# Performance work log

Measured on AMD Instinct MI355X. Metric: run time of the kernel, lower is better.

## Reference

```python
import jax, jax.numpy as jnp
import numpy as np

B, S, D, H = 2, 2048, 1024, 16
DK = D // H


def setup_inputs() -> dict:
    key = jax.random.key(0)
    ks = jax.random.split(key, 8)
    w_scale = 1.0 / np.sqrt(D)
    return {
        "query": jax.random.normal(ks[0], (B, S, D), jnp.float32),
        "key": jax.random.normal(ks[1], (B, S, D), jnp.float32),
        "value": jax.random.normal(ks[2], (B, S, D), jnp.float32),
        "Wq": jax.random.normal(ks[3], (D, D), jnp.float32) * w_scale,
        "bq": jnp.zeros((D,), jnp.float32),
        "Wk": jax.random.normal(ks[4], (D, D), jnp.float32) * w_scale,
        "bk": jnp.zeros((D,), jnp.float32),
        "Wv": jax.random.normal(ks[5], (D, D), jnp.float32) * w_scale,
        "bv": jnp.zeros((D,), jnp.float32),
        "Wo": jax.random.normal(ks[6], (D, D), jnp.float32) * w_scale,
        "bo": jnp.zeros((D,), jnp.float32),
    }


def _heads(x, W, b):
    # torch nn.Linear: y = x @ W.T + b ; then [B,S,D] -> [B,H,S,DK]
    y = x @ W.T + b
    return y.reshape(x.shape[0], x.shape[1], H, DK).transpose(0, 2, 1, 3)


def reference(query, key, value, Wq, bq, Wk, bk, Wv, bv, Wo, bo):
    q = _heads(query, Wq, bq)   # [B,H,S,DK]
    k = _heads(key, Wk, bk)
    v = _heads(value, Wv, bv)
    scale = 100.0 / np.sqrt(DK).astype(np.float32)
    scores = jnp.einsum("bhqd,bhkd->bhqk", q, k) * scale  # [B,H,Sq,Sk]
    prob = jax.nn.softmax(scores, axis=-1)                 # dropout p=0 -> identity
    out = jnp.einsum("bhqk,bhkd->bhqd", prob, v)           # [B,H,Sq,DK]
    mean_atp = prob.mean(axis=(1, 2))                      # mean over heads & query -> [B,Sk]
    out = out.transpose(0, 2, 1, 3).reshape(query.shape[0], -1, D)
    out = out @ Wo.T + bo
    return out, mean_atp
```

## Files before the change

### kernel.cpp

```cpp
#include <hip/hip_runtime.h>
#include <hip/hip_bf16.h>


#define B_  2
#define S_  2048
#define D_  1024
#define H_  16
#define DK_ 64

typedef __bf16 bf16x8 __attribute__((ext_vector_type(8)));
typedef float f32x4  __attribute__((ext_vector_type(4)));

__device__ __forceinline__ void ld_g2l16(const __bf16* g, __bf16* l) {
  __builtin_amdgcn_global_load_lds(
      (const __attribute__((address_space(1))) void*)g,
      (__attribute__((address_space(3))) void*)l, 16, 0, 0);
}

__device__ __forceinline__ void split3_body(const float* __restrict__ x,
                                            __bf16* __restrict__ y,
                                            int lbid, int tid, int mode)
{
  int i = (lbid * 256 + tid) * 8;
  float4 a = *(const float4*)(x + i);
  float4 b = *(const float4*)(x + i + 4);
  float xs[8] = {a.x, a.y, a.z, a.w, b.x, b.y, b.z, b.w};
  __bf16 out[24];
#pragma unroll
  for (int j = 0; j < 8; j++) {
    float v = xs[j];
    __bf16 hi = (__bf16)v;
    __bf16 lo = (__bf16)(v - (float)hi);
    if (mode == 0) { out[3*j] = hi; out[3*j+1] = hi; out[3*j+2] = lo; }
    else           { out[3*j] = hi; out[3*j+1] = lo; out[3*j+2] = hi; }
  }
  *(bf16x8*)(y + 3 * (size_t)i)      = *(bf16x8*)&out[0];
  *(bf16x8*)(y + 3 * (size_t)i + 8)  = *(bf16x8*)&out[8];
  *(bf16x8*)(y + 3 * (size_t)i + 16) = *(bf16x8*)&out[16];
}

__device__ __forceinline__ void tobf16_body(const float* __restrict__ x,
                                            __bf16* __restrict__ y,
                                            int lbid, int tid)
{
  int i = (lbid * 256 + tid) * 8;
  float4 a = *(const float4*)(x + i);
  float4 b = *(const float4*)(x + i + 4);
  __bf16 out[8] = {(__bf16)a.x, (__bf16)a.y, (__bf16)a.z, (__bf16)a.w,
                   (__bf16)b.x, (__bf16)b.y, (__bf16)b.z, (__bf16)b.w};
  *(bf16x8*)(y + i) = *(bf16x8*)&out[0];
}

__global__ __launch_bounds__(256)
void convert_all(const float* __restrict__ query, const float* __restrict__ key_,
                 const float* __restrict__ value, const float* __restrict__ Wq,
                 const float* __restrict__ Wk, const float* __restrict__ Wv,
                 const float* __restrict__ Wo, __bf16* __restrict__ qcat3,
                 __bf16* __restrict__ kcat3, __bf16* __restrict__ vxb,
                 __bf16* __restrict__ wqc3, __bf16* __restrict__ wkc3,
                 __bf16* __restrict__ wvb, __bf16* __restrict__ wob)
{
  int bid = blockIdx.x, tid = threadIdx.x;
  if (bid < 2048)       split3_body(query, qcat3, bid, tid, 0);
  else if (bid < 4096)  split3_body(key_,  kcat3, bid - 2048, tid, 0);
  else if (bid < 6144)  tobf16_body(value, vxb,   bid - 4096, tid);
  else if (bid < 6656)  split3_body(Wq, wqc3, bid - 6144, tid, 1);
  else if (bid < 7168)  split3_body(Wk, wkc3, bid - 6656, tid, 1);
  else if (bid < 7680)  tobf16_body(Wv, wvb, bid - 7168, tid);
  else                  tobf16_body(Wo, wob, bid - 7680, tid);
}

#define TM 64
#define TN 128
#define TK 64

__global__ __launch_bounds__(256)
void gemm_mfma(const __bf16* __restrict__ X, const __bf16* __restrict__ W,
               const float* __restrict__ bias, void* __restrict__ Y,
               void* __restrict__ Y2, int M, int N, int K, int out_mode,
               float osf)
{
  __shared__ __align__(16) __bf16 Xa[TM * TK];
  __shared__ __align__(16) __bf16 Wb[TN * TK];

  const int tid  = threadIdx.x;
  const int lane = tid & 63;
  const int w    = tid >> 6;
  const int c    = lane & 15;
  const int quad = lane >> 4;
  const int row0 = blockIdx.y * TM;
  const int col0 = blockIdx.x * TN;
  const int wc   = w * 32;

  f32x4 acc[4][2];
#pragma unroll
  for (int i = 0; i < 4; i++)
#pragma unroll
    for (int j = 0; j < 2; j++) acc[i][j] = (f32x4){0.f, 0.f, 0.f, 0.f};

  for (int k0 = 0; k0 < K; k0 += TK) {
    __syncthreads();
#pragma unroll
    for (int i = 0; i < 2; i++) {
      int chunk = i * 256 + w * 64 + lane;
      int r = chunk >> 3, dch = chunk & 7;
      ld_g2l16(X + (size_t)(row0 + r) * K + k0 + dch * 8, &Xa[chunk * 8]);
    }
#pragma unroll
    for (int i = 0; i < 4; i++) {
      int chunk = i * 256 + w * 64 + lane;
      int r = chunk >> 3, dch = chunk & 7;
      ld_g2l16(W + (size_t)(col0 + r) * K + k0 + dch * 8, &Wb[chunk * 8]);
    }
    __syncthreads();

#pragma unroll
    for (int cc = 0; cc < 2; cc++) {
      bf16x8 af[4], bf[2];
#pragma unroll
      for (int i = 0; i < 4; i++)
        af[i] = *(const bf16x8*)&Xa[(i * 16 + c) * TK + cc * 32 + quad * 8];
#pragma unroll
      for (int j = 0; j < 2; j++)
        bf[j] = *(const bf16x8*)&Wb[(wc + j * 16 + c) * TK + cc * 32 + quad * 8];
#pragma unroll
      for (int i = 0; i < 4; i++)
#pragma unroll
        for (int j = 0; j < 2; j++)
          acc[i][j] = __builtin_amdgcn_mfma_f32_16x16x32_bf16(af[i], bf[j],
                                                              acc[i][j], 0, 0, 0);
    }
  }

#pragma unroll
  for (int i = 0; i < 4; i++) {
#pragma unroll
    for (int j = 0; j < 2; j++) {
      int col = col0 + wc + j * 16 + c;
      float bcol = bias[col];
#pragma unroll
      for (int r = 0; r < 4; r++) {
        int row = row0 + i * 16 + quad * 4 + r;
        float v = (acc[i][j][r] + bcol) * osf;
        if (out_mode == 0) {
          ((float*)Y)[(size_t)row * N + col] = v;
        } else {
          int b2 = row >> 11, s = row & (S_ - 1);
          int h = col >> 6, dk = col & 63;
          if (out_mode == 1) {
            size_t off = ((size_t)(b2 * H_ + h) * S_ + s) * DK_ + dk;
            __bf16 hi = (__bf16)v;
            ((__bf16*)Y)[off]  = hi;
            ((__bf16*)Y2)[off] = (__bf16)(v - (float)hi);
          } else {
            ((__bf16*)Y)[((size_t)(b2 * H_ + h) * DK_ + dk) * S_ + s] = (__bf16)v;
          }
        }
      }
    }
  }
}

#define LSTR 72
#define PSTR 68

__device__ __forceinline__ void qk_scores(const __bf16* __restrict__ Kh,
                                          const __bf16* __restrict__ Kl,
                                          const bf16x8 qhf[2][2],
                                          const bf16x8 qlf[2][2],
                                          int c, int quad, f32x4 sc[2][4])
{
#pragma unroll
  for (int nt = 0; nt < 4; nt++) {
#pragma unroll
    for (int rg = 0; rg < 2; rg++) sc[rg][nt] = (f32x4){0.f, 0.f, 0.f, 0.f};
#pragma unroll
    for (int cc = 0; cc < 2; cc++) {
      bf16x8 bh8 = *(const bf16x8*)&Kh[(nt * 16 + c) * LSTR + cc * 32 + quad * 8];
      bf16x8 bl8 = *(const bf16x8*)&Kl[(nt * 16 + c) * LSTR + cc * 32 + quad * 8];
#pragma unroll
      for (int rg = 0; rg < 2; rg++) {
        sc[rg][nt] = __builtin_amdgcn_mfma_f32_16x16x32_bf16(qhf[rg][cc], bh8,
                                                             sc[rg][nt], 0, 0, 0);
        sc[rg][nt] = __builtin_amdgcn_mfma_f32_16x16x32_bf16(qhf[rg][cc], bl8,
                                                             sc[rg][nt], 0, 0, 0);
        sc[rg][nt] = __builtin_amdgcn_mfma_f32_16x16x32_bf16(qlf[rg][cc], bh8,
                                                             sc[rg][nt], 0, 0, 0);
      }
    }
  }
}

__global__ __launch_bounds__(256)
void attn_mfma(const __bf16* __restrict__ qh_ws, const __bf16* __restrict__ ql_ws,
               const __bf16* __restrict__ kh_ws, const __bf16* __restrict__ kl_ws,
               const __bf16* __restrict__ vt_ws, __bf16* __restrict__ attn_out,
               float* __restrict__ atp_out)
{
  __shared__ __align__(16) __bf16 Kh[64 * LSTR];
  __shared__ __align__(16) __bf16 Kl[64 * LSTR];
  __shared__ __align__(16) __bf16 Vt[64 * LSTR];
  __shared__ __align__(16) float  Ps[4][16 * PSTR];
  __shared__ float  atp_lds[S_];

  const int tid  = threadIdx.x;
  const int lane = tid & 63;
  const int w    = tid >> 6;
  const int c    = lane & 15;
  const int quad = lane >> 4;
  const int qb   = blockIdx.x;
  const int h    = blockIdx.y;
  const int b    = blockIdx.z;

  const size_t bh = (size_t)(b * H_ + h);
  const __bf16* qhg = qh_ws + (bh * S_ + qb * 128) * DK_;
  const __bf16* qlg = ql_ws + (bh * S_ + qb * 128) * DK_;
  const __bf16* khg = kh_ws + bh * S_ * DK_;
  const __bf16* klg = kl_ws + bh * S_ * DK_;
  const __bf16* vg  = vt_ws + bh * DK_ * S_;

  bf16x8 qhf[2][2], qlf[2][2];
#pragma unroll
  for (int rg = 0; rg < 2; rg++) {
    const __bf16* qrow = qhg + (size_t)(w * 32 + rg * 16 + c) * DK_;
    qhf[rg][0] = *(const bf16x8*)(qrow + quad * 8);
    qhf[rg][1] = *(const bf16x8*)(qrow + 32 + quad * 8);
    const __bf16* qrow2 = qlg + (size_t)(w * 32 + rg * 16 + c) * DK_;
    qlf[rg][0] = *(const bf16x8*)(qrow2 + quad * 8);
    qlf[rg][1] = *(const bf16x8*)(qrow2 + 32 + quad * 8);
  }

  float m_r[2][4], l_r[2][4];
#pragma unroll
  for (int rg = 0; rg < 2; rg++)
#pragma unroll
    for (int r = 0; r < 4; r++) { m_r[rg][r] = -1e30f; l_r[rg][r] = 0.f; }

  for (int kt = 0; kt < S_ / 64; kt++) {
    __syncthreads();
#pragma unroll
    for (int i = 0; i < 2; i++) {
      int idx = i * 256 + tid;
      int key = idx >> 3, dch = idx & 7;
      *(bf16x8*)&Kh[key * LSTR + dch * 8] =
          *(const bf16x8*)(khg + (size_t)(kt * 64 + key) * DK_ + dch * 8);
      *(bf16x8*)&Kl[key * LSTR + dch * 8] =
          *(const bf16x8*)(klg + (size_t)(kt * 64 + key) * DK_ + dch * 8);
    }
    __syncthreads();

    f32x4 sc[2][4];
    qk_scores(Kh, Kl, qhf, qlf, c, quad, sc);

    float tm[2][4], psum[2][4];
#pragma unroll
    for (int rg = 0; rg < 2; rg++)
#pragma unroll
      for (int r = 0; r < 4; r++)
        tm[rg][r] = fmaxf(fmaxf(sc[rg][0][r], sc[rg][1][r]),
                          fmaxf(sc[rg][2][r], sc[rg][3][r]));
#pragma unroll
    for (int o = 1; o < 16; o <<= 1)
#pragma unroll
      for (int rg = 0; rg < 2; rg++)
#pragma unroll
        for (int r = 0; r < 4; r++)
          tm[rg][r] = fmaxf(tm[rg][r], __shfl_xor(tm[rg][r], o, 64));

#pragma unroll
    for (int rg = 0; rg < 2; rg++)
#pragma unroll
      for (int r = 0; r < 4; r++) {
        float mnew = fmaxf(m_r[rg][r], tm[rg][r]);
        float p = 0.f;
#pragma unroll
        for (int nt = 0; nt < 4; nt++) p += exp2f(sc[rg][nt][r] - mnew);
        psum[rg][r] = p;
        l_r[rg][r] *= exp2f(m_r[rg][r] - mnew);
        m_r[rg][r] = mnew;
      }
#pragma unroll
    for (int o = 1; o < 16; o <<= 1)
#pragma unroll
      for (int rg = 0; rg < 2; rg++)
#pragma unroll
        for (int r = 0; r < 4; r++)
          psum[rg][r] += __shfl_xor(psum[rg][r], o, 64);
#pragma unroll
    for (int rg = 0; rg < 2; rg++)
#pragma unroll
      for (int r = 0; r < 4; r++) l_r[rg][r] += psum[rg][r];
  }

  float rl[2][4];
#pragma unroll
  for (int rg = 0; rg < 2; rg++)
#pragma unroll
    for (int r = 0; r < 4; r++) rl[rg][r] = 1.0f / l_r[rg][r];

  for (int i = tid; i < S_; i += 256) atp_lds[i] = 0.f;

  f32x4 of[2][4];
#pragma unroll
  for (int rg = 0; rg < 2; rg++)
#pragma unroll
    for (int nt = 0; nt < 4; nt++) of[rg][nt] = (f32x4){0.f, 0.f, 0.f, 0.f};

  float* ps = Ps[w];

  for (int kt = 0; kt < S_ / 64; kt++) {
    __syncthreads();
#pragma unroll
    for (int i = 0; i < 2; i++) {
      int idx = i * 256 + tid;
      int key = idx >> 3, dch = idx & 7;
      *(bf16x8*)&Kh[key * LSTR + dch * 8] =
          *(const bf16x8*)(khg + (size_t)(kt * 64 + key) * DK_ + dch * 8);
      *(bf16x8*)&Kl[key * LSTR + dch * 8] =
          *(const bf16x8*)(klg + (size_t)(kt * 64 + key) * DK_ + dch * 8);
      *(bf16x8*)&Vt[key * LSTR + dch * 8] =
          *(const bf16x8*)(vg + (size_t)key * S_ + kt * 64 + dch * 8);
    }
    __syncthreads();

    f32x4 sc[2][4];
    qk_scores(Kh, Kl, qhf, qlf, c, quad, sc);

    float t[4] = {0.f, 0.f, 0.f, 0.f};
#pragma unroll
    for (int rg = 0; rg < 2; rg++) {
#pragma unroll
      for (int nt = 0; nt < 4; nt++)
#pragma unroll
        for (int r = 0; r < 4; r++) {
          float p = exp2f(sc[rg][nt][r] - m_r[rg][r]) * rl[rg][r];
          ps[(quad * 4 + r) * PSTR + nt * 16 + c] = p;
          t[nt] += p;
        }
      bf16x8 pa[2];
#pragma unroll
      for (int cc = 0; cc < 2; cc++) {
        const float* pp = &ps[c * PSTR + cc * 32 + quad * 8];
        f32x4 p0 = *(const f32x4*)pp;
        f32x4 p1 = *(const f32x4*)(pp + 4);
        bf16x8 v8;
#pragma unroll
        for (int j = 0; j < 4; j++) { v8[j] = (__bf16)p0[j]; v8[4 + j] = (__bf16)p1[j]; }
        pa[cc] = v8;
      }
#pragma unroll
      for (int nt = 0; nt < 4; nt++)
#pragma unroll
        for (int cc = 0; cc < 2; cc++) {
          bf16x8 vb = *(const bf16x8*)&Vt[(nt * 16 + c) * LSTR + cc * 32 + quad * 8];
          of[rg][nt] = __builtin_amdgcn_mfma_f32_16x16x32_bf16(pa[cc], vb,
                                                               of[rg][nt], 0, 0, 0);
        }
    }

#pragma unroll
    for (int nt = 0; nt < 4; nt++) {
      float tt = t[nt];
      tt += __shfl_xor(tt, 16, 64);
      tt += __shfl_xor(tt, 32, 64);
      if (quad == 0) atomicAdd(&atp_lds[kt * 64 + nt * 16 + c], tt);
    }
  }

#pragma unroll
  for (int rg = 0; rg < 2; rg++)
#pragma unroll
    for (int nt = 0; nt < 4; nt++)
#pragma unroll
      for (int r = 0; r < 4; r++)
        attn_out[((size_t)(b * S_ + qb * 128 + w * 32 + rg * 16 + quad * 4 + r)) * D_
                 + h * DK_ + nt * 16 + c] = (__bf16)of[rg][nt][r];

  __syncthreads();
  const float inv = 1.0f / ((float)H_ * (float)S_);
  for (int i = tid; i < S_; i += 256)
    atomicAdd(&atp_out[b * S_ + i], atp_lds[i] * inv);
}

__global__ void zero_f32(float* __restrict__ p, int n) {
  int i = blockIdx.x * 256 + threadIdx.x;
  if (i < n) p[i] = 0.f;
}

extern "C" void kernel_launch(void* const* d_in, const int* in_sizes, int n_in,
                              void* d_out, int out_size, void* d_ws, size_t ws_size,
                              hipStream_t stream)
{
  const float* query = (const float*)d_in[0];
  const float* key_  = (const float*)d_in[1];
  const float* value = (const float*)d_in[2];
  const float* Wq = (const float*)d_in[3];
  const float* bq = (const float*)d_in[4];
  const float* Wk = (const float*)d_in[5];
  const float* bk = (const float*)d_in[6];
  const float* Wv = (const float*)d_in[7];
  const float* bv = (const float*)d_in[8];
  const float* Wo = (const float*)d_in[9];
  const float* bo = (const float*)d_in[10];

  float* out = (float*)d_out;
  float* atp = out + (size_t)B_ * S_ * D_;

  const size_t NE = (size_t)B_ * S_ * D_;
  const size_t NW = (size_t)D_ * D_;
  __bf16* p = (__bf16*)d_ws;
  __bf16* qcat3 = p;               p += 3 * NE;
  __bf16* kcat3 = p;               p += 3 * NE;
  __bf16* wqc3  = p;               p += 3 * NW;
  __bf16* wkc3  = p;               p += 3 * NW;
  __bf16* vxb   = p;               p += NE;
  __bf16* wvb   = p;               p += NW;
  __bf16* wob   = p;               p += NW;
  __bf16* qh_ws = p;               p += NE;
  __bf16* ql_ws = p;               p += NE;
  __bf16* kh_ws = p;               p += NE;
  __bf16* kl_ws = p;               p += NE;
  __bf16* vt_ws = kcat3;
  __bf16* a_ws  = qcat3;

  const int M = B_ * S_;
  const float QSF = 18.0337320f;

  convert_all<<<8192, 256, 0, stream>>>(query, key_, value, Wq, Wk, Wv, Wo,
                                        qcat3, kcat3, vxb, wqc3, wkc3, wvb, wob);

  dim3 ggrid(D_ / TN, M / TM);
  gemm_mfma<<<ggrid, 256, 0, stream>>>(qcat3, wqc3, bq, qh_ws, ql_ws, M, D_, 3 * D_, 1, QSF);
  gemm_mfma<<<ggrid, 256, 0, stream>>>(kcat3, wkc3, bk, kh_ws, kl_ws, M, D_, 3 * D_, 1, 1.0f);
  gemm_mfma<<<ggrid, 256, 0, stream>>>(vxb,   wvb,  bv, vt_ws, nullptr, M, D_, D_, 2, 1.0f);

  zero_f32<<<(B_ * S_ + 255) / 256, 256, 0, stream>>>(atp, B_ * S_);

  attn_mfma<<<dim3(S_ / 128, H_, B_), 256, 0, stream>>>(qh_ws, ql_ws, kh_ws, kl_ws,
                                                        vt_ws, a_ws, atp);

  gemm_mfma<<<ggrid, 256, 0, stream>>>(a_ws, wob, bo, out, nullptr, M, D_, D_, 0, 1.0f);
}
```

Before: 511.3 us.

## Merge QKV GEMMs into one launch, fold atp zeroing, use 8-wave attention blocks

```diff
diff --git a/kernel.cpp b/kernel.cpp
--- a/kernel.cpp
+++ b/kernel.cpp
@@ -58,7 +58,8 @@
                  const float* __restrict__ Wo, __bf16* __restrict__ qcat3,
                  __bf16* __restrict__ kcat3, __bf16* __restrict__ vxb,
                  __bf16* __restrict__ wqc3, __bf16* __restrict__ wkc3,
-                 __bf16* __restrict__ wvb, __bf16* __restrict__ wob)
+                 __bf16* __restrict__ wvb, __bf16* __restrict__ wob,
+                 float* __restrict__ atp)
 {
   int bid = blockIdx.x, tid = threadIdx.x;
   if (bid < 2048)       split3_body(query, qcat3, bid, tid, 0);
@@ -67,29 +68,31 @@
   else if (bid < 6656)  split3_body(Wq, wqc3, bid - 6144, tid, 1);
   else if (bid < 7168)  split3_body(Wk, wkc3, bid - 6656, tid, 1);
   else if (bid < 7680)  tobf16_body(Wv, wvb, bid - 7168, tid);
-  else                  tobf16_body(Wo, wob, bid - 7680, tid);
+  else if (bid < 8192)  tobf16_body(Wo, wob, bid - 7680, tid);
+  else {
+    int base = (bid - 8192) * 2048;
+#pragma unroll
+    for (int j = 0; j < 8; j++) atp[base + j * 256 + tid] = 0.f;
+  }
 }
 
 #define TM 64
 #define TN 128
 #define TK 64
 
-__global__ __launch_bounds__(256)
-void gemm_mfma(const __bf16* __restrict__ X, const __bf16* __restrict__ W,
+__device__ __forceinline__
+void gemm_body(const __bf16* __restrict__ X, const __bf16* __restrict__ W,
                const float* __restrict__ bias, void* __restrict__ Y,
-               void* __restrict__ Y2, int M, int N, int K, int out_mode,
-               float osf)
-{
-  __shared__ __align__(16) __bf16 Xa[TM * TK];
-  __shared__ __align__(16) __bf16 Wb[TN * TK];
-
+               void* __restrict__ Y2, int N, int K, int out_mode, float osf,
+               __bf16* Xa, __bf16* Wb, int bx, int by)
+{
   const int tid  = threadIdx.x;
   const int lane = tid & 63;
   const int w    = tid >> 6;
   const int c    = lane & 15;
   const int quad = lane >> 4;
-  const int row0 = blockIdx.y * TM;
-  const int col0 = blockIdx.x * TN;
+  const int row0 = by * TM;
+  const int col0 = bx * TN;
   const int wc   = w * 32;
 
   f32x4 acc[4][2];
@@ -161,37 +164,60 @@
   }
 }
 
+__global__ __launch_bounds__(256)
+void gemm_qkv(const __bf16* __restrict__ qcat3, const __bf16* __restrict__ wqc3,
+              const float* __restrict__ bq, __bf16* __restrict__ qh, __bf16* __restrict__ ql,
+              const __bf16* __restrict__ kcat3, const __bf16* __restrict__ wkc3,
+              const float* __restrict__ bk, __bf16* __restrict__ kh, __bf16* __restrict__ kl,
+              const __bf16* __restrict__ vxb, const __bf16* __restrict__ wvb,
+              const float* __restrict__ bv, __bf16* __restrict__ vt, float qsf)
+{
+  __shared__ __align__(16) __bf16 Xa[TM * TK];
+  __shared__ __align__(16) __bf16 Wb[TN * TK];
+  int z = blockIdx.z;
+  if (z == 0)
+    gemm_body(qcat3, wqc3, bq, qh, ql, D_, 3 * D_, 1, qsf, Xa, Wb, blockIdx.x, blockIdx.y);
+  else if (z == 1)
+    gemm_body(kcat3, wkc3, bk, kh, kl, D_, 3 * D_, 1, 1.0f, Xa, Wb, blockIdx.x, blockIdx.y);
+  else
+    gemm_body(vxb, wvb, bv, vt, nullptr, D_, D_, 2, 1.0f, Xa, Wb, blockIdx.x, blockIdx.y);
+}
+
+__global__ __launch_bounds__(256)
+void gemm_mfma(const __bf16* __restrict__ X, const __bf16* __restrict__ W,
+               const float* __restrict__ bias, void* __restrict__ Y,
+               void* __restrict__ Y2, int M, int N, int K, int out_mode,
+               float osf)
+{
+  __shared__ __align__(16) __bf16 Xa[TM * TK];
+  __shared__ __align__(16) __bf16 Wb[TN * TK];
+  gemm_body(X, W, bias, Y, Y2, N, K, out_mode, osf, Xa, Wb, blockIdx.x, blockIdx.y);
+}
+
 #define LSTR 72
 #define PSTR 68
 
 __device__ __forceinline__ void qk_scores(const __bf16* __restrict__ Kh,
                                           const __bf16* __restrict__ Kl,
-                                          const bf16x8 qhf[2][2],
-                                          const bf16x8 qlf[2][2],
-                                          int c, int quad, f32x4 sc[2][4])
+                                          const bf16x8 qhf[2],
+                                          const bf16x8 qlf[2],
+                                          int c, int quad, f32x4 sc[4])
 {
 #pragma unroll
   for (int nt = 0; nt < 4; nt++) {
-#pragma unroll
-    for (int rg = 0; rg < 2; rg++) sc[rg][nt] = (f32x4){0.f, 0.f, 0.f, 0.f};
+    sc[nt] = (f32x4){0.f, 0.f, 0.f, 0.f};
 #pragma unroll
     for (int cc = 0; cc < 2; cc++) {
       bf16x8 bh8 = *(const bf16x8*)&Kh[(nt * 16 + c) * LSTR + cc * 32 + quad * 8];
       bf16x8 bl8 = *(const bf16x8*)&Kl[(nt * 16 + c) * LSTR + cc * 32 + quad * 8];
-#pragma unroll
-      for (int rg = 0; rg < 2; rg++) {
-        sc[rg][nt] = __builtin_amdgcn_mfma_f32_16x16x32_bf16(qhf[rg][cc], bh8,
-                                                             sc[rg][nt], 0, 0, 0);
-        sc[rg][nt] = __builtin_amdgcn_mfma_f32_16x16x32_bf16(qhf[rg][cc], bl8,
-                                                             sc[rg][nt], 0, 0, 0);
-        sc[rg][nt] = __builtin_amdgcn_mfma_f32_16x16x32_bf16(qlf[rg][cc], bh8,
-                                                             sc[rg][nt], 0, 0, 0);
-      }
-    }
-  }
-}
-
-__global__ __launch_bounds__(256)
+      sc[nt] = __builtin_amdgcn_mfma_f32_16x16x32_bf16(qhf[cc], bh8, sc[nt], 0, 0, 0);
+      sc[nt] = __builtin_amdgcn_mfma_f32_16x16x32_bf16(qhf[cc], bl8, sc[nt], 0, 0, 0);
+      sc[nt] = __builtin_amdgcn_mfma_f32_16x16x32_bf16(qlf[cc], bh8, sc[nt], 0, 0, 0);
+    }
+  }
+}
+
+__global__ __launch_bounds__(512)
 void attn_mfma(const __bf16* __restrict__ qh_ws, const __bf16* __restrict__ ql_ws,
                const __bf16* __restrict__ kh_ws, const __bf16* __restrict__ kl_ws,
                const __bf16* __restrict__ vt_ws, __bf16* __restrict__ attn_out,
@@ -200,7 +226,7 @@
   __shared__ __align__(16) __bf16 Kh[64 * LSTR];
   __shared__ __align__(16) __bf16 Kl[64 * LSTR];
   __shared__ __align__(16) __bf16 Vt[64 * LSTR];
-  __shared__ __align__(16) float  Ps[4][16 * PSTR];
+  __shared__ __align__(16) float  Ps[8][16 * PSTR];
   __shared__ float  atp_lds[S_];
 
   const int tid  = threadIdx.x;
@@ -219,29 +245,24 @@
   const __bf16* klg = kl_ws + bh * S_ * DK_;
   const __bf16* vg  = vt_ws + bh * DK_ * S_;
 
-  bf16x8 qhf[2][2], qlf[2][2];
-#pragma unroll
-  for (int rg = 0; rg < 2; rg++) {
-    const __bf16* qrow = qhg + (size_t)(w * 32 + rg * 16 + c) * DK_;
-    qhf[rg][0] = *(const bf16x8*)(qrow + quad * 8);
-    qhf[rg][1] = *(const bf16x8*)(qrow + 32 + quad * 8);
-    const __bf16* qrow2 = qlg + (size_t)(w * 32 + rg * 16 + c) * DK_;
-    qlf[rg][0] = *(const bf16x8*)(qrow2 + quad * 8);
-    qlf[rg][1] = *(const bf16x8*)(qrow2 + 32 + quad * 8);
-  }
-
-  float m_r[2][4], l_r[2][4];
-#pragma unroll
-  for (int rg = 0; rg < 2; rg++)
-#pragma unroll
-    for (int r = 0; r < 4; r++) { m_r[rg][r] = -1e30f; l_r[rg][r] = 0.f; }
+  bf16x8 qhf[2], qlf[2];
+  {
+    const __bf16* qrow = qhg + (size_t)(w * 16 + c) * DK_;
+    qhf[0] = *(const bf16x8*)(qrow + quad * 8);
+    qhf[1] = *(const bf16x8*)(qrow + 32 + quad * 8);
+    const __bf16* qrow2 = qlg + (size_t)(w * 16 + c) * DK_;
+    qlf[0] = *(const bf16x8*)(qrow2 + quad * 8);
+    qlf[1] = *(const bf16x8*)(qrow2 + 32 + quad * 8);
+  }
+
+  float m_r[4], l_r[4];
+#pragma unroll
+  for (int r = 0; r < 4; r++) { m_r[r] = -1e30f; l_r[r] = 0.f; }
 
   for (int kt = 0; kt < S_ / 64; kt++) {
     __syncthreads();
-#pragma unroll
-    for (int i = 0; i < 2; i++) {
-      int idx = i * 256 + tid;
-      int key = idx >> 3, dch = idx & 7;
+    {
+      int key = tid >> 3, dch = tid & 7;
       *(bf16x8*)&Kh[key * LSTR + dch * 8] =
           *(const bf16x8*)(khg + (size_t)(kt * 64 + key) * DK_ + dch * 8);
       *(bf16x8*)&Kl[key * LSTR + dch * 8] =
@@ -249,71 +270,54 @@
     }
     __syncthreads();
 
-    f32x4 sc[2][4];
+    f32x4 sc[4];
     qk_scores(Kh, Kl, qhf, qlf, c, quad, sc);
 
-    float tm[2][4], psum[2][4];
-#pragma unroll
-    for (int rg = 0; rg < 2; rg++)
+    float tm[4], psum[4];
+#pragma unroll
+    for (int r = 0; r < 4; r++)
+      tm[r] = fmaxf(fmaxf(sc[0][r], sc[1][r]), fmaxf(sc[2][r], sc[3][r]));
+#pragma unroll
+    for (int o = 1; o < 16; o <<= 1)
 #pragma unroll
       for (int r = 0; r < 4; r++)
-        tm[rg][r] = fmaxf(fmaxf(sc[rg][0][r], sc[rg][1][r]),
-                          fmaxf(sc[rg][2][r], sc[rg][3][r]));
+        tm[r] = fmaxf(tm[r], __shfl_xor(tm[r], o, 64));
+
+#pragma unroll
+    for (int r = 0; r < 4; r++) {
+      float mnew = fmaxf(m_r[r], tm[r]);
+      float p = 0.f;
+#pragma unroll
+      for (int nt = 0; nt < 4; nt++) p += exp2f(sc[nt][r] - mnew);
+      psum[r] = p;
+      l_r[r] *= exp2f(m_r[r] - mnew);
+      m_r[r] = mnew;
+    }
 #pragma unroll
     for (int o = 1; o < 16; o <<= 1)
 #pragma unroll
-      for (int rg = 0; rg < 2; rg++)
-#pragma unroll
-        for (int r = 0; r < 4; r++)
-          tm[rg][r] = fmaxf(tm[rg][r], __shfl_xor(tm[rg][r], o, 64));
-
-#pragma unroll
-    for (int rg = 0; rg < 2; rg++)
-#pragma unroll
-      for (int r = 0; r < 4; r++) {
-        float mnew = fmaxf(m_r[rg][r], tm[rg][r]);
-        float p = 0.f;
-#pragma unroll
-        for (int nt = 0; nt < 4; nt++) p += exp2f(sc[rg][nt][r] - mnew);
-        psum[rg][r] = p;
-        l_r[rg][r] *= exp2f(m_r[rg][r] - mnew);
-        m_r[rg][r] = mnew;
-      }
-#pragma unroll
-    for (int o = 1; o < 16; o <<= 1)
-#pragma unroll
-      for (int rg = 0; rg < 2; rg++)
-#pragma unroll
-        for (int r = 0; r < 4; r++)
-          psum[rg][r] += __shfl_xor(psum[rg][r], o, 64);
-#pragma unroll
-    for (int rg = 0; rg < 2; rg++)
-#pragma unroll
-      for (int r = 0; r < 4; r++) l_r[rg][r] += psum[rg][r];
-  }
-
-  float rl[2][4];
-#pragma unroll
-  for (int rg = 0; rg < 2; rg++)
-#pragma unroll
-    for (int r = 0; r < 4; r++) rl[rg][r] = 1.0f / l_r[rg][r];
-
-  for (int i = tid; i < S_; i += 256) atp_lds[i] = 0.f;
-
-  f32x4 of[2][4];
-#pragma unroll
-  for (int rg = 0; rg < 2; rg++)
-#pragma unroll
-    for (int nt = 0; nt < 4; nt++) of[rg][nt] = (f32x4){0.f, 0.f, 0.f, 0.f};
+      for (int r = 0; r < 4; r++)
+        psum[r] += __shfl_xor(psum[r], o, 64);
+#pragma unroll
+    for (int r = 0; r < 4; r++) l_r[r] += psum[r];
+  }
+
+  float z_r[4];
+#pragma unroll
+  for (int r = 0; r < 4; r++) z_r[r] = m_r[r] + log2f(l_r[r]);
+
+  for (int i = tid; i < S_; i += 512) atp_lds[i] = 0.f;
+
+  f32x4 of[4];
+#pragma unroll
+  for (int nt = 0; nt < 4; nt++) of[nt] = (f32x4){0.f, 0.f, 0.f, 0.f};
 
   float* ps = Ps[w];
 
   for (int kt = 0; kt < S_ / 64; kt++) {
     __syncthreads();
-#pragma unroll
-    for (int i = 0; i < 2; i++) {
-      int idx = i * 256 + tid;
-      int key = idx >> 3, dch = idx & 7;
+    {
+      int key = tid >> 3, dch = tid & 7;
       *(bf16x8*)&Kh[key * LSTR + dch * 8] =
           *(const bf16x8*)(khg + (size_t)(kt * 64 + key) * DK_ + dch * 8);
       *(bf16x8*)&Kl[key * LSTR + dch * 8] =
@@ -323,40 +327,39 @@
     }
     __syncthreads();
 
-    f32x4 sc[2][4];
+    f32x4 sc[4];
     qk_scores(Kh, Kl, qhf, qlf, c, quad, sc);
 
-    float t[4] = {0.f, 0.f, 0.f, 0.f};
-#pragma unroll
-    for (int rg = 0; rg < 2; rg++) {
-#pragma unroll
-      for (int nt = 0; nt < 4; nt++)
-#pragma unroll
-        for (int r = 0; r < 4; r++) {
-          float p = exp2f(sc[rg][nt][r] - m_r[rg][r]) * rl[rg][r];
-          ps[(quad * 4 + r) * PSTR + nt * 16 + c] = p;
-          t[nt] += p;
-        }
-      bf16x8 pa[2];
+    float t[4];
+#pragma unroll
+    for (int nt = 0; nt < 4; nt++) {
+      t[nt] = 0.f;
+#pragma unroll
+      for (int r = 0; r < 4; r++) {
+        float p = exp2f(sc[nt][r] - z_r[r]);
+        ps[(quad * 4 + r) * PSTR + nt * 16 + c] = p;
+        t[nt] += p;
+      }
+    }
+
+    bf16x8 pa[2];
+#pragma unroll
+    for (int cc = 0; cc < 2; cc++) {
+      const float* pp = &ps[c * PSTR + cc * 32 + quad * 8];
+      f32x4 p0 = *(const f32x4*)pp;
+      f32x4 p1 = *(const f32x4*)(pp + 4);
+      bf16x8 v8;
+#pragma unroll
+      for (int j = 0; j < 4; j++) { v8[j] = (__bf16)p0[j]; v8[4 + j] = (__bf16)p1[j]; }
+      pa[cc] = v8;
+    }
+#pragma unroll
+    for (int nt = 0; nt < 4; nt++)
 #pragma unroll
       for (int cc = 0; cc < 2; cc++) {
-        const float* pp = &ps[c * PSTR + cc * 32 + quad * 8];
-        f32x4 p0 = *(const f32x4*)pp;
-        f32x4 p1 = *(const f32x4*)(pp + 4);
-        bf16x8 v8;
-#pragma unroll
-        for (int j = 0; j < 4; j++) { v8[j] = (__bf16)p0[j]; v8[4 + j] = (__bf16)p1[j]; }
-        pa[cc] = v8;
+        bf16x8 vb = *(const bf16x8*)&Vt[(nt * 16 + c) * LSTR + cc * 32 + quad * 8];
+        of[nt] = __builtin_amdgcn_mfma_f32_16x16x32_bf16(pa[cc], vb, of[nt], 0, 0, 0);
       }
-#pragma unroll
-      for (int nt = 0; nt < 4; nt++)
-#pragma unroll
-        for (int cc = 0; cc < 2; cc++) {
-          bf16x8 vb = *(const bf16x8*)&Vt[(nt * 16 + c) * LSTR + cc * 32 + quad * 8];
-          of[rg][nt] = __builtin_amdgcn_mfma_f32_16x16x32_bf16(pa[cc], vb,
-                                                               of[rg][nt], 0, 0, 0);
-        }
-    }
 
 #pragma unroll
     for (int nt = 0; nt < 4; nt++) {
@@ -368,23 +371,16 @@
   }
 
 #pragma unroll
-  for (int rg = 0; rg < 2; rg++)
-#pragma unroll
-    for (int nt = 0; nt < 4; nt++)
-#pragma unroll
-      for (int r = 0; r < 4; r++)
-        attn_out[((size_t)(b * S_ + qb * 128 + w * 32 + rg * 16 + quad * 4 + r)) * D_
-                 + h * DK_ + nt * 16 + c] = (__bf16)of[rg][nt][r];
+  for (int nt = 0; nt < 4; nt++)
+#pragma unroll
+    for (int r = 0; r < 4; r++)
+      attn_out[((size_t)(b * S_ + qb * 128 + w * 16 + quad * 4 + r)) * D_
+               + h * DK_ + nt * 16 + c] = (__bf16)of[nt][r];
 
   __syncthreads();
   const float inv = 1.0f / ((float)H_ * (float)S_);
-  for (int i = tid; i < S_; i += 256)
+  for (int i = tid; i < S_; i += 512)
     atomicAdd(&atp_out[b * S_ + i], atp_lds[i] * inv);
-}
-
-__global__ void zero_f32(float* __restrict__ p, int n) {
-  int i = blockIdx.x * 256 + threadIdx.x;
-  if (i < n) p[i] = 0.f;
 }
 
 extern "C" void kernel_launch(void* const* d_in, const int* in_sizes, int n_in,
@@ -426,18 +422,18 @@
   const int M = B_ * S_;
   const float QSF = 18.0337320f;
 
-  convert_all<<<8192, 256, 0, stream>>>(query, key_, value, Wq, Wk, Wv, Wo,
-                                        qcat3, kcat3, vxb, wqc3, wkc3, wvb, wob);
-
-  dim3 ggrid(D_ / TN, M / TM);
-  gemm_mfma<<<ggrid, 256, 0, stream>>>(qcat3, wqc3, bq, qh_ws, ql_ws, M, D_, 3 * D_, 1, QSF);
-  gemm_mfma<<<ggrid, 256, 0, stream>>>(kcat3, wkc3, bk, kh_ws, kl_ws, M, D_, 3 * D_, 1, 1.0f);
-  gemm_mfma<<<ggrid, 256, 0, stream>>>(vxb,   wvb,  bv, vt_ws, nullptr, M, D_, D_, 2, 1.0f);
-
-  zero_f32<<<(B_ * S_ + 255) / 256, 256, 0, stream>>>(atp, B_ * S_);
-
-  attn_mfma<<<dim3(S_ / 128, H_, B_), 256, 0, stream>>>(qh_ws, ql_ws, kh_ws, kl_ws,
+  convert_all<<<8194, 256, 0, stream>>>(query, key_, value, Wq, Wk, Wv, Wo,
+                                        qcat3, kcat3, vxb, wqc3, wkc3, wvb, wob,
+                                        atp);
+
+  gemm_qkv<<<dim3(D_ / TN, M / TM, 3), 256, 0, stream>>>(
+      qcat3, wqc3, bq, qh_ws, ql_ws,
+      kcat3, wkc3, bk, kh_ws, kl_ws,
+      vxb,   wvb,  bv, vt_ws, QSF);
+
+  attn_mfma<<<dim3(S_ / 128, H_, B_), 512, 0, stream>>>(qh_ws, ql_ws, kh_ws, kl_ws,
                                                         vt_ws, a_ws, atp);
 
-  gemm_mfma<<<ggrid, 256, 0, stream>>>(a_ws, wob, bo, out, nullptr, M, D_, D_, 0, 1.0f);
-}
+  gemm_mfma<<<dim3(D_ / TN, M / TM), 256, 0, stream>>>(a_ws, wob, bo, out, nullptr,
+                                                       M, D_, D_, 0, 1.0f);
+}
```

Result: faster. 480.7 us (-6.0%).
